# Optimization experiments

Hardware: AMD Instinct MI355X
Metric: run time of the kernel (lower is better)

Reference implementation:

```python
import jax, jax.numpy as jnp
import numpy as np

N = 50000   # nodes
E = 100000  # edges
C = 256     # in_channels


def setup_inputs() -> dict:
    key = jax.random.key(0)
    k1, k2, k3, k4 = jax.random.split(key, 4)
    x = jax.random.normal(k1, (N, C), dtype=jnp.float32)
    edge_index = jax.random.randint(k2, (2, E), 0, N, dtype=jnp.int32)
    # torch nn.Linear default init ~ U(-1/sqrt(C), 1/sqrt(C)); exact dist irrelevant for correctness
    bound = 1.0 / np.sqrt(C)
    W = jax.random.uniform(k3, (C, C), minval=-bound, maxval=bound, dtype=jnp.float32)
    b = jax.random.uniform(k4, (C,), minval=-bound, maxval=bound, dtype=jnp.float32)
    return {"x": x, "edge_index": edge_index, "W": W, "b": b}


def _scatter_mean_with_self_loops(xt, edge_index, n):
    # edge_index_sl = [edges ; self-loops]
    ar = jnp.arange(n, dtype=edge_index.dtype)
    src = jnp.concatenate([edge_index[0], ar])  # [E+N]
    dst = jnp.concatenate([edge_index[1], ar])  # [E+N]
    gathered = xt[src]                           # [E+N, C]
    sums = jax.ops.segment_sum(gathered, dst, num_segments=n)
    cnt = jax.ops.segment_sum(jnp.ones_like(dst, dtype=xt.dtype), dst, num_segments=n)
    # every node has a self-loop so cnt >= 1; guard anyway
    return sums / jnp.maximum(cnt, 1.0)[:, None]


def _merge_edges(edge_index, n):
    # Sequential greedy edge merge, faithful to the Python loop, as a lax.scan.
    remaining0 = jnp.ones((n,), dtype=jnp.int32)
    discarded0 = jnp.zeros((n,), dtype=jnp.int32).at[edge_index[0]].set(1)

    def step(carry, st):
        rem, disc = carry
        s, t = st[0], st[1]
        cond = (rem[s] == 1) & (rem[t] == 1) & (disc[t] == 1) & (s != t)
        rem = rem.at[s].set(jnp.where(cond, 0, rem[s]))
        disc = disc.at[t].set(jnp.where(cond, 0, disc[t]))
        return (rem, disc), None

    (remaining, _), _ = jax.lax.scan(step, (remaining0, discarded0), edge_index.T)
    return remaining  # int32 0/1 mask, 1 = kept node


def reference(x, edge_index, W, b):
    n = x.shape[0]
    xt = x @ W.T + b                                   # self.trans(x)
    h = _scatter_mean_with_self_loops(xt, edge_index, n)  # [N, C]
    mask = _merge_edges(edge_index, n)                 # nodes_remaining
    # Original returns h[mask == 1] (data-dependent shape). For jit-compatibility
    # we return h with dropped rows zeroed, plus the mask; compaction is a
    # trivial post-processing gather.
    out = h * mask.astype(h.dtype)[:, None]
    return out, mask
```

## Files before the change

kernel.cpp:

```cpp
#include <hip/hip_runtime.h>
#include <hip/hip_bf16.h>

#define C_DIM 256

#define MBLK 64
#define MTHR 1024
#define MT_TOT (MBLK * MTHR)
#define MEPT 2
#define EPOCH0 2000u
#define MAXR 1900
#define GROWS 128

typedef __attribute__((ext_vector_type(8))) short bf16x8;
typedef __attribute__((ext_vector_type(4))) float f32x4;

__device__ __forceinline__ unsigned short f32_to_bf16(float f) {
    __hip_bfloat16 h = __float2bfloat16(f);
    return __builtin_bit_cast(unsigned short, h);
}
__device__ __forceinline__ float bf16_to_f32(unsigned short u) {
    unsigned v = ((unsigned)u) << 16;
    return __builtin_bit_cast(float, v);
}
__device__ __forceinline__ unsigned ld_ag(const unsigned* p) {
    return __hip_atomic_load(p, __ATOMIC_RELAXED, __HIP_MEMORY_SCOPE_AGENT);
}
__device__ __forceinline__ unsigned long long ld_ag8(const unsigned* p) {
    return __hip_atomic_load((const unsigned long long*)p, __ATOMIC_RELAXED, __HIP_MEMORY_SCOPE_AGENT);
}
__device__ __forceinline__ void st_ag(unsigned* p, unsigned v) {
    __hip_atomic_store(p, v, __ATOMIC_RELAXED, __HIP_MEMORY_SCOPE_AGENT);
}

__global__ __launch_bounds__(256) void prep(const float* __restrict__ W,
                                            unsigned short* __restrict__ W_bf,
                                            const int* __restrict__ esrc,
                                            const int* __restrict__ edst,
                                            unsigned char* __restrict__ disc0,
                                            int* __restrict__ cnt,
                                            unsigned short* __restrict__ slots,
                                            int E) {
    int tid = blockIdx.x * blockDim.x + threadIdx.x;
    int T = gridDim.x * blockDim.x;
    for (int i = tid; i < C_DIM * C_DIM; i += T) W_bf[i] = f32_to_bf16(W[i]);
    for (int e = tid; e < E; e += T) {
        int s = esrc[e], t = edst[e];
        disc0[s] = 1;
        int pos = atomicAdd(&cnt[t], 1);
        if (pos < 32) slots[(size_t)t * 32 + pos] = (unsigned short)s;
    }
}

__global__ __launch_bounds__(1024) void fused_kernel(
    const float* __restrict__ X, const unsigned short* __restrict__ W_bf,
    const float* __restrict__ bias, unsigned short* __restrict__ xt_bf,
    const int* __restrict__ esrc, const int* __restrict__ edst,
    const unsigned char* __restrict__ disc0,
    unsigned* __restrict__ mins, unsigned* __restrict__ bar,
    float* __restrict__ remf, int E, int N) {
    __shared__ unsigned short Xs[GROWS][136];

    if (blockIdx.x >= MBLK) {
        const int i0 = (int)(blockIdx.x - MBLK) * GROWS;
        const int tid = threadIdx.x;
        const int w = tid >> 6, l = tid & 63;
        const int wr = w >> 2, wc = w & 3;
        const int lr = l & 15, lkq = l >> 4;
        f32x4 acc[2][4] = {};

        for (int h = 0; h < 2; ++h) {
            const int k0 = h * 128;
            __syncthreads();
            for (int idx = tid; idx < GROWS * 32; idx += MTHR) {
                int row = idx >> 5, c4 = idx & 31;
                int gi = i0 + row;
                float4 v = make_float4(0.f, 0.f, 0.f, 0.f);
                if (gi < N) v = *(const float4*)&X[(size_t)gi * C_DIM + k0 + c4 * 4];
                ushort4 u;
                u.x = f32_to_bf16(v.x); u.y = f32_to_bf16(v.y);
                u.z = f32_to_bf16(v.z); u.w = f32_to_bf16(v.w);
                *(ushort4*)&Xs[row][c4 * 4] = u;
            }
            __syncthreads();
#pragma unroll
            for (int r = 0; r < 4; ++r) {
                bf16x8 a[2];
#pragma unroll
                for (int ai = 0; ai < 2; ++ai)
                    a[ai] = *(const bf16x8*)&Xs[wr * 32 + ai * 16 + lr][r * 32 + lkq * 8];
#pragma unroll
                for (int bj = 0; bj < 4; ++bj) {
                    int col = wc * 64 + bj * 16 + lr;
                    bf16x8 b = *(const bf16x8*)(W_bf + (size_t)col * C_DIM + k0 + r * 32 + lkq * 8);
#pragma unroll
                    for (int ai = 0; ai < 2; ++ai)
                        acc[ai][bj] = __builtin_amdgcn_mfma_f32_16x16x32_bf16(a[ai], b, acc[ai][bj], 0, 0, 0);
                }
            }
        }
#pragma unroll
        for (int bj = 0; bj < 4; ++bj) {
            int col = wc * 64 + bj * 16 + lr;
            float bv = bias[col];
#pragma unroll
            for (int ai = 0; ai < 2; ++ai) {
#pragma unroll
                for (int q = 0; q < 4; ++q) {
                    int row = i0 + wr * 32 + ai * 16 + lkq * 4 + q;
                    if (row < N)
                        xt_bf[(size_t)row * C_DIM + col] = f32_to_bf16(acc[ai][bj][q] + bv);
                }
            }
        }
        return;
    }

    __shared__ unsigned ldsAny;
    __shared__ unsigned ldsChg;
    const int gtid = blockIdx.x * MTHR + threadIdx.x;
    const int tid = threadIdx.x;

    int es[MEPT], ts[MEPT];
    bool cand[MEPT], fire[MEPT];
#pragma unroll
    for (int i = 0; i < MEPT; ++i) {
        int e = gtid + i * MT_TOT;
        es[i] = 0; ts[i] = 0; cand[i] = false;
        if (e < E) {
            es[i] = esrc[e]; ts[i] = edst[e];
            cand[i] = (es[i] != ts[i]) && (disc0[ts[i]] != 0);
        }
        fire[i] = cand[i];
    }
    if (tid == 0) ldsAny = 0;
    __syncthreads();

    unsigned gen = 0;
    unsigned prevAny = 1;
    int r = 0;
    while (true) {
        if (r > 0) {
            unsigned tagP = (EPOCH0 - (unsigned)(r - 1)) << 20;
            const unsigned* pm = mins + (size_t)((r - 1) & 1) * 2 * N;
            bool anych = false;
#pragma unroll
            for (int i = 0; i < MEPT; ++i) {
                if (cand[i]) {
                    unsigned e = (unsigned)(gtid + i * MT_TOT);
                    unsigned va = ld_ag(&pm[2 * es[i]]);
                    unsigned long long p8 = ld_ag8(&pm[2 * ts[i]]);
                    unsigned vb = (unsigned)p8;
                    unsigned vc = (unsigned)(p8 >> 32);
                    bool blk = ((va - tagP) < e) | ((vb - tagP) < e) | ((vc - tagP) < e);
                    bool nf = !blk;
                    anych |= (nf != fire[i]);
                    fire[i] = nf;
                }
            }
            if (anych) ldsAny = 1;
        }
        {
            unsigned tagC = (EPOCH0 - (unsigned)r) << 20;
            unsigned* cm = mins + (size_t)(r & 1) * 2 * N;
#pragma unroll
            for (int i = 0; i < MEPT; ++i) {
                if (fire[i]) {
                    unsigned e = (unsigned)(gtid + i * MT_TOT);
                    atomicMin(&cm[2 * es[i]], tagC | e);
                    atomicMin(&cm[2 * ts[i] + 1], tagC | e);
                }
            }
        }
        __syncthreads();
        unsigned blockAny = (r == 0) ? 1u : ldsAny;
        ++gen;

        if (tid == 0) {
            unsigned bits = (r == 0) ? 3u
                          : ((blockAny << (r & 1)) | (prevAny << ((r - 1) & 1)));
            __hip_atomic_store(&bar[blockIdx.x * 16], (gen << 2) | bits,
                               __ATOMIC_RELEASE, __HIP_MEMORY_SCOPE_AGENT);
            ldsAny = 0;
        }
        if (tid < 64) {
            unsigned target = gen << 2;
            unsigned v;
            for (;;) {
                v = __hip_atomic_load(&bar[tid * 16], __ATOMIC_RELAXED, __HIP_MEMORY_SCOPE_AGENT);
                if ((int)(v - target) >= 0) break;
                __builtin_amdgcn_s_sleep(1);
            }
            __threadfence();
            unsigned chg = ((v >> (r & 1)) & 1) ? 1u : 0u;
            unsigned long long bl = __ballot(chg != 0);
            if (tid == 0) ldsChg = (bl != 0ull) ? 1u : 0u;
        }
        __syncthreads();
        unsigned globalChg = ldsChg;
        prevAny = blockAny;
        if (r > 0 && globalChg == 0) break;
        if (r >= MAXR) break;
        ++r;
    }

    unsigned tagF = (EPOCH0 - (unsigned)r) << 20;
    const unsigned* fm = mins + (size_t)(r & 1) * 2 * N;
    for (int x = gtid; x < N; x += MT_TOT) {
        unsigned v = ld_ag(&fm[2 * x]);
        remf[x] = ((v - tagF) < (1u << 20)) ? 0.f : 1.f;
    }
}

__global__ __launch_bounds__(256) void pool(const unsigned short* __restrict__ xt_bf,
                                            const int* __restrict__ cnt,
                                            const unsigned short* __restrict__ slots,
                                            const float* __restrict__ remf,
                                            float* __restrict__ out, int N) {
    int wv = threadIdx.x >> 6, lane = threadIdx.x & 63;
    int node = blockIdx.x * 4 + wv;
    if (node >= N) return;
    int deg = cnt[node];
    float m = remf[node];
    float inv = m / (float)(deg + 1);
    int dl = deg > 32 ? 32 : deg;
    unsigned long long sl4 = *(const unsigned long long*)&slots[(size_t)node * 32];
    ushort4 u = ((const ushort4*)(xt_bf + (size_t)node * C_DIM))[lane];
    float s0 = bf16_to_f32(u.x), s1 = bf16_to_f32(u.y);
    float s2 = bf16_to_f32(u.z), s3 = bf16_to_f32(u.w);
    int dl4 = dl > 4 ? 4 : dl;
#pragma unroll 4
    for (int j = 0; j < dl4; ++j) {
        int src = (int)((sl4 >> (16 * j)) & 0xFFFFull);
        ushort4 v = ((const ushort4*)(xt_bf + (size_t)src * C_DIM))[lane];
        s0 += bf16_to_f32(v.x); s1 += bf16_to_f32(v.y);
        s2 += bf16_to_f32(v.z); s3 += bf16_to_f32(v.w);
    }
    for (int j = 4; j < dl; ++j) {
        int src = slots[(size_t)node * 32 + j];
        ushort4 v = ((const ushort4*)(xt_bf + (size_t)src * C_DIM))[lane];
        s0 += bf16_to_f32(v.x); s1 += bf16_to_f32(v.y);
        s2 += bf16_to_f32(v.z); s3 += bf16_to_f32(v.w);
    }
    float4 o = make_float4(s0 * inv, s1 * inv, s2 * inv, s3 * inv);
    *(float4*)&out[(size_t)node * C_DIM + lane * 4] = o;
    if (lane == 0) out[(size_t)N * C_DIM + node] = m;
}

extern "C" void kernel_launch(void* const* d_in, const int* in_sizes, int n_in,
                              void* d_out, int out_size, void* d_ws, size_t ws_size,
                              hipStream_t stream) {
    const float* X = (const float*)d_in[0];
    const int* EI = (const int*)d_in[1];
    const float* W = (const float*)d_in[2];
    const float* bias = (const float*)d_in[3];
    const int N = in_sizes[0] / C_DIM;
    const int E = in_sizes[1] / 2;
    const int* esrc = EI;
    const int* edst = EI + E;
    float* out = (float*)d_out;

    char* p = (char*)d_ws;
    auto take = [&](size_t bytes) {
        char* q = p;
        p += (bytes + 255) & ~(size_t)255;
        return q;
    };
    unsigned short* xt_bf = (unsigned short*)take((size_t)N * C_DIM * 2);
    unsigned short* W_bf  = (unsigned short*)take((size_t)C_DIM * C_DIM * 2);
    int* cnt              = (int*)take((size_t)N * 4);
    unsigned short* slots = (unsigned short*)take((size_t)N * 32 * 2);
    unsigned* mins        = (unsigned*)take((size_t)4 * N * 4);
    float* remf           = (float*)take((size_t)N * 4);
    unsigned char* disc0  = (unsigned char*)take((size_t)N);
    unsigned* bar         = (unsigned*)take((size_t)MBLK * 16 * 4);
    (void)ws_size; (void)n_in; (void)out_size;

    hipMemsetAsync(disc0, 0, N, stream);
    hipMemsetAsync(cnt, 0, (size_t)N * 4, stream);

    prep<<<256, 256, 0, stream>>>(W, W_bf, esrc, edst, disc0, cnt, slots, E);

    int nGemm = (N + GROWS - 1) / GROWS;
    fused_kernel<<<MBLK + nGemm, MTHR, 0, stream>>>(X, W_bf, bias, xt_bf,
                                                    esrc, edst, disc0,
                                                    mins, bar, remf, E, N);

    pool<<<(N + 3) / 4, 256, 0, stream>>>(xt_bf, cnt, slots, remf, out, N);
}
```

Before: 252.9 us.

## Aggregate neighbors on raw X before GEMM, then zero masked rows

Relies on linearity: the mean of (xW^T+b) equals (mean x)W^T+b, so each GEMM block first gathers and averages neighbor rows of X in fp32 and runs the matmul on the pooled tile. The result goes straight to the fp32 output, which removes the bf16 xt intermediate and the separate pooling pass that re-read it. A light kernel then writes the mask column and zeroes the rows of dropped nodes. The trade-off is that the gathers now read fp32 X, twice the bytes of bf16 xt, and they run inside the GEMM blocks with a larger shared-memory tile, which may reduce occupancy.

Result: no change. 248.0 us (-1.9%).

```diff
diff --git a/kernel.cpp b/kernel.cpp
--- a/kernel.cpp
+++ b/kernel.cpp
@@ -27,9 +27,6 @@
 }
 __device__ __forceinline__ unsigned long long ld_ag8(const unsigned* p) {
     return __hip_atomic_load((const unsigned long long*)p, __ATOMIC_RELAXED, __HIP_MEMORY_SCOPE_AGENT);
-}
-__device__ __forceinline__ void st_ag(unsigned* p, unsigned v) {
-    __hip_atomic_store(p, v, __ATOMIC_RELAXED, __HIP_MEMORY_SCOPE_AGENT);
 }
 
 __global__ __launch_bounds__(256) void prep(const float* __restrict__ W,
@@ -53,51 +50,70 @@
 
 __global__ __launch_bounds__(1024) void fused_kernel(
     const float* __restrict__ X, const unsigned short* __restrict__ W_bf,
-    const float* __restrict__ bias, unsigned short* __restrict__ xt_bf,
+    const float* __restrict__ bias, float* __restrict__ out,
+    const int* __restrict__ cnt, const unsigned short* __restrict__ slots,
     const int* __restrict__ esrc, const int* __restrict__ edst,
     const unsigned char* __restrict__ disc0,
     unsigned* __restrict__ mins, unsigned* __restrict__ bar,
     float* __restrict__ remf, int E, int N) {
-    __shared__ unsigned short Xs[GROWS][136];
+    __shared__ unsigned short Xs[GROWS][264];
 
     if (blockIdx.x >= MBLK) {
         const int i0 = (int)(blockIdx.x - MBLK) * GROWS;
         const int tid = threadIdx.x;
         const int w = tid >> 6, l = tid & 63;
+
+        for (int nn = 0; nn < 8; ++nn) {
+            int lrow = w * 8 + nn;
+            int node = i0 + lrow;
+            float4 s = make_float4(0.f, 0.f, 0.f, 0.f);
+            if (node < N) {
+                s = *(const float4*)&X[(size_t)node * C_DIM + l * 4];
+                int deg = cnt[node];
+                int dl = deg > 32 ? 32 : deg;
+                const unsigned short* sl = slots + (size_t)node * 32;
+                unsigned long long sl4 = *(const unsigned long long*)sl;
+                int dl4 = dl > 4 ? 4 : dl;
+#pragma unroll 4
+                for (int j = 0; j < dl4; ++j) {
+                    int src = (int)((sl4 >> (16 * j)) & 0xFFFFull);
+                    float4 v = *(const float4*)&X[(size_t)src * C_DIM + l * 4];
+                    s.x += v.x; s.y += v.y; s.z += v.z; s.w += v.w;
+                }
+                for (int j = 4; j < dl; ++j) {
+                    int src = sl[j];
+                    float4 v = *(const float4*)&X[(size_t)src * C_DIM + l * 4];
+                    s.x += v.x; s.y += v.y; s.z += v.z; s.w += v.w;
+                }
+                float inv = 1.f / (float)(deg + 1);
+                s.x *= inv; s.y *= inv; s.z *= inv; s.w *= inv;
+            }
+            ushort4 u;
+            u.x = f32_to_bf16(s.x); u.y = f32_to_bf16(s.y);
+            u.z = f32_to_bf16(s.z); u.w = f32_to_bf16(s.w);
+            *(ushort4*)&Xs[lrow][l * 4] = u;
+        }
+        __syncthreads();
+
         const int wr = w >> 2, wc = w & 3;
         const int lr = l & 15, lkq = l >> 4;
         f32x4 acc[2][4] = {};
-
-        for (int h = 0; h < 2; ++h) {
-            const int k0 = h * 128;
-            __syncthreads();
-            for (int idx = tid; idx < GROWS * 32; idx += MTHR) {
-                int row = idx >> 5, c4 = idx & 31;
-                int gi = i0 + row;
-                float4 v = make_float4(0.f, 0.f, 0.f, 0.f);
-                if (gi < N) v = *(const float4*)&X[(size_t)gi * C_DIM + k0 + c4 * 4];
-                ushort4 u;
-                u.x = f32_to_bf16(v.x); u.y = f32_to_bf16(v.y);
-                u.z = f32_to_bf16(v.z); u.w = f32_to_bf16(v.w);
-                *(ushort4*)&Xs[row][c4 * 4] = u;
-            }
-            __syncthreads();
-#pragma unroll
-            for (int r = 0; r < 4; ++r) {
-                bf16x8 a[2];
+#pragma unroll
+        for (int r = 0; r < 8; ++r) {
+            bf16x8 a[2];
+#pragma unroll
+            for (int ai = 0; ai < 2; ++ai)
+                a[ai] = *(const bf16x8*)&Xs[wr * 32 + ai * 16 + lr][r * 32 + lkq * 8];
+#pragma unroll
+            for (int bj = 0; bj < 4; ++bj) {
+                int col = wc * 64 + bj * 16 + lr;
+                bf16x8 b = *(const bf16x8*)(W_bf + (size_t)col * C_DIM + r * 32 + lkq * 8);
 #pragma unroll
                 for (int ai = 0; ai < 2; ++ai)
-                    a[ai] = *(const bf16x8*)&Xs[wr * 32 + ai * 16 + lr][r * 32 + lkq * 8];
-#pragma unroll
-                for (int bj = 0; bj < 4; ++bj) {
-                    int col = wc * 64 + bj * 16 + lr;
-                    bf16x8 b = *(const bf16x8*)(W_bf + (size_t)col * C_DIM + k0 + r * 32 + lkq * 8);
-#pragma unroll
-                    for (int ai = 0; ai < 2; ++ai)
-                        acc[ai][bj] = __builtin_amdgcn_mfma_f32_16x16x32_bf16(a[ai], b, acc[ai][bj], 0, 0, 0);
-                }
-            }
-        }
+                    acc[ai][bj] = __builtin_amdgcn_mfma_f32_16x16x32_bf16(a[ai], b, acc[ai][bj], 0, 0, 0);
+            }
+        }
+
 #pragma unroll
         for (int bj = 0; bj < 4; ++bj) {
             int col = wc * 64 + bj * 16 + lr;
@@ -108,7 +124,7 @@
                 for (int q = 0; q < 4; ++q) {
                     int row = i0 + wr * 32 + ai * 16 + lkq * 4 + q;
                     if (row < N)
-                        xt_bf[(size_t)row * C_DIM + col] = f32_to_bf16(acc[ai][bj][q] + bv);
+                        out[(size_t)row * C_DIM + col] = acc[ai][bj][q] + bv;
                 }
             }
         }
@@ -211,39 +227,17 @@
     }
 }
 
-__global__ __launch_bounds__(256) void pool(const unsigned short* __restrict__ xt_bf,
-                                            const int* __restrict__ cnt,
-                                            const unsigned short* __restrict__ slots,
-                                            const float* __restrict__ remf,
-                                            float* __restrict__ out, int N) {
+__global__ __launch_bounds__(256) void mask_zero(const float* __restrict__ remf,
+                                                 float* __restrict__ out, int N) {
     int wv = threadIdx.x >> 6, lane = threadIdx.x & 63;
     int node = blockIdx.x * 4 + wv;
     if (node >= N) return;
-    int deg = cnt[node];
     float m = remf[node];
-    float inv = m / (float)(deg + 1);
-    int dl = deg > 32 ? 32 : deg;
-    unsigned long long sl4 = *(const unsigned long long*)&slots[(size_t)node * 32];
-    ushort4 u = ((const ushort4*)(xt_bf + (size_t)node * C_DIM))[lane];
-    float s0 = bf16_to_f32(u.x), s1 = bf16_to_f32(u.y);
-    float s2 = bf16_to_f32(u.z), s3 = bf16_to_f32(u.w);
-    int dl4 = dl > 4 ? 4 : dl;
-#pragma unroll 4
-    for (int j = 0; j < dl4; ++j) {
-        int src = (int)((sl4 >> (16 * j)) & 0xFFFFull);
-        ushort4 v = ((const ushort4*)(xt_bf + (size_t)src * C_DIM))[lane];
-        s0 += bf16_to_f32(v.x); s1 += bf16_to_f32(v.y);
-        s2 += bf16_to_f32(v.z); s3 += bf16_to_f32(v.w);
-    }
-    for (int j = 4; j < dl; ++j) {
-        int src = slots[(size_t)node * 32 + j];
-        ushort4 v = ((const ushort4*)(xt_bf + (size_t)src * C_DIM))[lane];
-        s0 += bf16_to_f32(v.x); s1 += bf16_to_f32(v.y);
-        s2 += bf16_to_f32(v.z); s3 += bf16_to_f32(v.w);
-    }
-    float4 o = make_float4(s0 * inv, s1 * inv, s2 * inv, s3 * inv);
-    *(float4*)&out[(size_t)node * C_DIM + lane * 4] = o;
     if (lane == 0) out[(size_t)N * C_DIM + node] = m;
+    if (m == 0.f) {
+        float4 z = make_float4(0.f, 0.f, 0.f, 0.f);
+        *(float4*)&out[(size_t)node * C_DIM + lane * 4] = z;
+    }
 }
 
 extern "C" void kernel_launch(void* const* d_in, const int* in_sizes, int n_in,
@@ -265,7 +259,6 @@
         p += (bytes + 255) & ~(size_t)255;
         return q;
     };
-    unsigned short* xt_bf = (unsigned short*)take((size_t)N * C_DIM * 2);
     unsigned short* W_bf  = (unsigned short*)take((size_t)C_DIM * C_DIM * 2);
     int* cnt              = (int*)take((size_t)N * 4);
     unsigned short* slots = (unsigned short*)take((size_t)N * 32 * 2);
@@ -281,9 +274,9 @@
     prep<<<256, 256, 0, stream>>>(W, W_bf, esrc, edst, disc0, cnt, slots, E);
 
     int nGemm = (N + GROWS - 1) / GROWS;
-    fused_kernel<<<MBLK + nGemm, MTHR, 0, stream>>>(X, W_bf, bias, xt_bf,
+    fused_kernel<<<MBLK + nGemm, MTHR, 0, stream>>>(X, W_bf, bias, out, cnt, slots,
                                                     esrc, edst, disc0,
                                                     mins, bar, remf, E, N);
 
-    pool<<<(N + 3) / 4, 256, 0, stream>>>(xt_bf, cnt, slots, remf, out, N);
-}
+    mask_zero<<<(N + 3) / 4, 256, 0, stream>>>(remf, out, N);
+}
```
